# Kernel tuning notes

Measured on AMD Instinct MI355X. Metric: run time of the kernel, lower is better.

Reference implementation:

```python
import jax, jax.numpy as jnp
import numpy as np
import math

FACTOR = 3.0

def setup_inputs() -> dict:
    key = jax.random.key(0)
    k1, k2, k3 = jax.random.split(key, 3)
    B, L, H, E = 16, 4096, 8, 64
    queries = jax.random.normal(k1, (B, L, H, E), dtype=jnp.float32)
    keys = jax.random.normal(k2, (B, L, H, E), dtype=jnp.float32)
    values = jax.random.normal(k3, (B, L, H, E), dtype=jnp.float32)
    return {"queries": queries, "keys": keys, "values": values}

def reference(queries, keys, values):
    B, L, H, E = queries.shape
    top_k = int(FACTOR * math.log(L))  # 24 for L=4096 (static)
    # [B,H,E,L] layout for FFT along time
    q = jnp.transpose(queries, (0, 2, 3, 1))
    k = jnp.transpose(keys, (0, 2, 3, 1))
    v = jnp.transpose(values, (0, 2, 3, 1))
    # period-based autocorrelation via FFT cross-correlation
    qf = jnp.fft.rfft(q, axis=-1)
    kf = jnp.fft.rfft(k, axis=-1)
    corr = jnp.fft.irfft(qf * jnp.conj(kf), n=L, axis=-1)  # [B,H,E,L]
    # training-mode aggregation: shared top-k delay indices across batch
    mean_value = corr.mean(axis=(1, 2))                # [B,L]
    _, index = jax.lax.top_k(mean_value.mean(axis=0), top_k)  # [top_k]
    weights = mean_value[:, index]                     # [B,top_k]
    tmp_corr = jax.nn.softmax(weights, axis=-1)        # [B,top_k]
    delays_agg = jnp.zeros_like(v)
    for i in range(top_k):  # small static loop over delays
        pattern = jnp.roll(v, -index[i], axis=-1)
        delays_agg = delays_agg + pattern * tmp_corr[:, i][:, None, None, None]
    V = jnp.transpose(delays_agg, (0, 3, 1, 2))        # [B,L,H,E]
    return V
```

## Files before the change

### kernel.cpp

```cpp
#include <hip/hip_runtime.h>
#include <math.h>

#define B_ 16
#define L_ 4096
#define H_ 8
#define E_ 64
#define C_ 512
#define K_ 24
#define NT 256
#define RPAD 257

__device__ __forceinline__ int br12(int x) { return (int)(__brev((unsigned)x) >> 20); }

__device__ __forceinline__ float2 cmul(float2 a, float2 b) {
    return make_float2(a.x * b.x - a.y * b.y, a.x * b.y + a.y * b.x);
}
__device__ __forceinline__ float2 cadd(float2 a, float2 b) { return make_float2(a.x + b.x, a.y + b.y); }
__device__ __forceinline__ float2 csub(float2 a, float2 b) { return make_float2(a.x - b.x, a.y - b.y); }

__device__ __forceinline__ void bar_lds() {
    asm volatile("s_waitcnt lgkmcnt(0)" ::: "memory");
    __builtin_amdgcn_s_barrier();
}

__device__ __forceinline__ void fft16(float2 a[16]) {
    const float r2 = 0.70710678118654752f;
    const float c1 = 0.92387953251128676f;
    const float s1 = 0.38268343236508977f;
    const float2 W16[8] = {
        make_float2(1.f, 0.f),  make_float2(c1, -s1),  make_float2(r2, -r2),  make_float2(s1, -c1),
        make_float2(0.f, -1.f), make_float2(-s1, -c1), make_float2(-r2, -r2), make_float2(-c1, -s1)};
    #pragma unroll
    for (int j = 0; j < 8; ++j) {
        float2 u = a[j], v = a[j + 8];
        a[j]     = cadd(u, v);
        a[j + 8] = cmul(csub(u, v), W16[j]);
    }
    #pragma unroll
    for (int b = 0; b < 16; b += 8)
        #pragma unroll
        for (int j = 0; j < 4; ++j) {
            float2 u = a[b + j], v = a[b + j + 4];
            a[b + j]     = cadd(u, v);
            a[b + j + 4] = cmul(csub(u, v), W16[2 * j]);
        }
    #pragma unroll
    for (int b = 0; b < 16; b += 4)
        #pragma unroll
        for (int j = 0; j < 2; ++j) {
            float2 u = a[b + j], v = a[b + j + 2];
            a[b + j]     = cadd(u, v);
            a[b + j + 2] = cmul(csub(u, v), W16[4 * j]);
        }
    #pragma unroll
    for (int b = 0; b < 16; b += 2) {
        float2 u = a[b], v = a[b + 1];
        a[b]     = cadd(u, v);
        a[b + 1] = csub(u, v);
    }
}

__global__ __launch_bounds__(256) void k_zero(float* __restrict__ p, int n) {
    int i = blockIdx.x * 256 + threadIdx.x;
    if (i < n) p[i] = 0.f;
}

__global__ __launch_bounds__(256) void k_transpose(const float* __restrict__ q,
                                                   const float* __restrict__ k,
                                                   float2* __restrict__ z,
                                                   int b0) {
    __shared__ float tq[64][65];
    __shared__ float tk[64][65];
    int bl = blockIdx.z;
    int b  = b0 + bl;
    int t0 = blockIdx.x * 64;
    int c0 = blockIdx.y * 64;
    int tid  = threadIdx.x;
    int row  = tid >> 4;
    int col4 = (tid & 15) << 2;
    const size_t base = (size_t)b * L_ * C_;
    #pragma unroll
    for (int p = 0; p < 4; ++p) {
        int rr = (p << 4) + row;
        size_t off = base + (size_t)(t0 + rr) * C_ + (c0 + col4);
        float4 q4 = *(const float4*)(q + off);
        float4 k4 = *(const float4*)(k + off);
        tq[rr][col4 + 0] = q4.x; tq[rr][col4 + 1] = q4.y;
        tq[rr][col4 + 2] = q4.z; tq[rr][col4 + 3] = q4.w;
        tk[rr][col4 + 0] = k4.x; tk[rr][col4 + 1] = k4.y;
        tk[rr][col4 + 2] = k4.z; tk[rr][col4 + 3] = k4.w;
    }
    __syncthreads();
    #pragma unroll
    for (int p = 0; p < 4; ++p) {
        int cc = (p << 4) + row;
        int tg = col4;
        float4 w0 = make_float4(tq[tg + 0][cc], tk[tg + 0][cc],
                                tq[tg + 1][cc], tk[tg + 1][cc]);
        float4 w1 = make_float4(tq[tg + 2][cc], tk[tg + 2][cc],
                                tq[tg + 3][cc], tk[tg + 3][cc]);
        size_t zoff = ((size_t)bl * C_ + (c0 + cc)) * L_ + (t0 + tg);
        *(float4*)&z[zoff]     = w0;
        *(float4*)&z[zoff + 2] = w1;
    }
}

__global__ __launch_bounds__(256) void k_fft_accum(const float2* __restrict__ z,
                                                   float* __restrict__ cross,
                                                   int b0) {
    __shared__ float2 s[16 * RPAD];
    __shared__ float2 tw256[256];
    const int br4[16] = {0, 8, 4, 12, 2, 10, 6, 14, 1, 9, 5, 13, 3, 11, 7, 15};
    int t  = threadIdx.x;
    int bl = blockIdx.y;
    int b  = b0 + bl;
    int c0 = blockIdx.x * 8;

    {
        int r1 = t >> 4, m2 = t & 15;
        float sn, cs;
        sincospif((float)(r1 * m2) / 128.0f, &sn, &cs);
        tw256[t] = make_float2(cs, -sn);
    }
    float2 twA[15];
    #pragma unroll
    for (int k1 = 1; k1 < 16; ++k1) {
        float sn, cs;
        sincospif((float)(t * k1) / 2048.0f, &sn, &cs);
        twA[k1 - 1] = make_float2(cs, -sn);
    }
    float accx[16], accy[16];
    #pragma unroll
    for (int r = 0; r < 16; ++r) { accx[r] = 0.f; accy[r] = 0.f; }

    float2 a[16];
    {
        const float2* zc0 = z + ((size_t)bl * C_ + c0) * L_;
        #pragma unroll
        for (int j = 0; j < 16; ++j) a[j] = zc0[(j << 8) + t];
    }
    bar_lds();

    const int rowB = t >> 4, m2B = t & 15;
    const int k1C = t & 15, r1C = t >> 4;

    for (int cc = 0; cc < 8; ++cc) {
        fft16(a);
        #pragma unroll
        for (int k1 = 0; k1 < 16; ++k1) {
            float2 v = a[br4[k1]];
            if (k1) v = cmul(v, twA[k1 - 1]);
            s[k1 * RPAD + t] = v;
        }
        __syncthreads();
        #pragma unroll
        for (int m1 = 0; m1 < 16; ++m1) a[m1] = s[rowB * RPAD + (m1 << 4) + m2B];
        fft16(a);
        #pragma unroll
        for (int r1 = 0; r1 < 16; ++r1) {
            float2 v = cmul(a[br4[r1]], tw256[(r1 << 4) + m2B]);
            s[rowB * RPAD + (r1 << 4) + m2B] = v;
        }
        __syncthreads();
        #pragma unroll
        for (int m2 = 0; m2 < 16; ++m2) a[m2] = s[k1C * RPAD + (r1C << 4) + m2];
        fft16(a);
        __syncthreads();
        #pragma unroll
        for (int r2 = 0; r2 < 16; ++r2)
            s[(r2 << 8) + (r1C << 4) + k1C] = a[br4[r2]];
        if (cc < 7) {
            const float2* zn = z + ((size_t)bl * C_ + (c0 + cc + 1)) * L_;
            #pragma unroll
            for (int j = 0; j < 16; ++j) a[j] = zn[(j << 8) + t];
        }
        bar_lds();
        #pragma unroll
        for (int r = 0; r < 16; ++r) {
            int p  = t + (r << 8);
            int pp = (L_ - p) & (L_ - 1);
            float2 A  = s[p];
            float2 Bv = s[pp];
            float Qr = 0.5f * (A.x + Bv.x);
            float Qi = 0.5f * (A.y - Bv.y);
            float Kr = 0.5f * (A.y + Bv.y);
            float Ki = 0.5f * (A.x - Bv.x);
            accx[r] += Qr * Kr - Qi * Ki;
            accy[r] += Qr * Ki + Qi * Kr;
        }
        bar_lds();
    }
    #pragma unroll
    for (int r = 0; r < 16; ++r) {
        int p = t + (r << 8);
        atomicAdd(&cross[((size_t)b * L_ + p) * 2 + 0], accx[r]);
        atomicAdd(&cross[((size_t)b * L_ + p) * 2 + 1], accy[r]);
    }
}

__global__ __launch_bounds__(256) void k_ifft(const float* __restrict__ cross,
                                              float* __restrict__ mv) {
    __shared__ float2 s[L_];
    __shared__ float2 tw[L_ / 2];
    int tid = threadIdx.x;
    int b   = blockIdx.x;
    for (int j = tid; j < L_ / 2; j += NT) {
        float sn, cs;
        sincospif((float)j / 2048.0f, &sn, &cs);
        tw[j] = make_float2(cs, -sn);
    }
    const float2* cr = (const float2*)cross;
    #pragma unroll
    for (int r = 0; r < 16; ++r) {
        int p = tid + (r << 8);
        s[p] = cr[(size_t)b * L_ + br12(p)];
    }
    __syncthreads();
    for (int m = 1; m <= 12; ++m) {
        int half = 1 << (m - 1);
        #pragma unroll
        for (int t8 = 0; t8 < 8; ++t8) {
            int t  = tid + (t8 << 8);
            int kk = t & (half - 1);
            int i0 = ((t >> (m - 1)) << m) | kk;
            int i1 = i0 + half;
            float2 a = s[i0], bb = s[i1];
            float2 w = tw[kk << (12 - m)];
            float bwx = bb.x * w.x + bb.y * w.y;
            float bwy = bb.y * w.x - bb.x * w.y;
            s[i0] = make_float2(a.x + bwx, a.y + bwy);
            s[i1] = make_float2(a.x - bwx, a.y - bwy);
        }
        __syncthreads();
    }
    const float scale = 1.0f / ((float)L_ * (float)C_);
    #pragma unroll
    for (int r = 0; r < 16; ++r) {
        int p = tid + (r << 8);
        mv[(size_t)b * L_ + p] = s[p].x * scale;
    }
}

__global__ __launch_bounds__(256) void k_topk(const float* __restrict__ mv,
                                              int* __restrict__ idx,
                                              float* __restrict__ wts) {
    __shared__ float wv[4];
    __shared__ int   wi[4];
    __shared__ int   idxL[K_];
    int tid = threadIdx.x;
    float vloc[16];
    #pragma unroll
    for (int r = 0; r < 16; ++r) {
        int tt = tid + (r << 8);
        float ssum = 0.f;
        for (int b = 0; b < B_; ++b) ssum += mv[(size_t)b * L_ + tt];
        vloc[r] = ssum;
    }
    int lane = tid & 63, w = tid >> 6;
    for (int i = 0; i < K_; ++i) {
        float best = -INFINITY; int bi = 1 << 30;
        #pragma unroll
        for (int r = 0; r < 16; ++r) {
            float v = vloc[r]; int ii = tid + (r << 8);
            if (v > best || (v == best && ii < bi)) { best = v; bi = ii; }
        }
        #pragma unroll
        for (int off = 32; off > 0; off >>= 1) {
            float ov = __shfl_down(best, off);
            int   oi = __shfl_down(bi, off);
            if (ov > best || (ov == best && oi < bi)) { best = ov; bi = oi; }
        }
        if (lane == 0) { wv[w] = best; wi[w] = bi; }
        __syncthreads();
        if (tid == 0) {
            float bb = wv[0]; int bj = wi[0];
            for (int j = 1; j < 4; ++j)
                if (wv[j] > bb || (wv[j] == bb && wi[j] < bj)) { bb = wv[j]; bj = wi[j]; }
            idxL[i] = bj; idx[i] = bj;
        }
        __syncthreads();
        int win = idxL[i];
        #pragma unroll
        for (int r = 0; r < 16; ++r)
            if (win == tid + (r << 8)) vloc[r] = -INFINITY;
    }
    if (tid < B_) {
        int b = tid;
        float ww[K_]; float wm = -INFINITY;
        for (int i = 0; i < K_; ++i) { ww[i] = mv[(size_t)b * L_ + idxL[i]]; wm = fmaxf(wm, ww[i]); }
        float ssum = 0.f;
        for (int i = 0; i < K_; ++i) { ww[i] = expf(ww[i] - wm); ssum += ww[i]; }
        float inv = 1.f / ssum;
        for (int i = 0; i < K_; ++i) wts[b * K_ + i] = ww[i] * inv;
    }
}

__global__ __launch_bounds__(256) void k_agg(const float* __restrict__ vals,
                                             const int* __restrict__ idx,
                                             const float* __restrict__ wts,
                                             float* __restrict__ out) {
    __shared__ float4 sv[L_];
    __shared__ int   di[K_];
    __shared__ float dw[K_];
    const int tid = threadIdx.x;
    int id = blockIdx.x;
    int wk = ((id & 7) << 8) | (id >> 3);
    int b  = wk >> 7;
    int c0 = (wk & 127) << 2;

    if (tid < K_) { di[tid] = idx[tid]; dw[tid] = wts[b * K_ + tid]; }

    const float* gbase = vals + (size_t)b * L_ * C_ + c0;
    #pragma unroll
    for (int it = 0; it < 16; ++it) {
        int tau = (it << 8) + tid;
        const float* g = gbase + (size_t)tau * C_;
        float4* l = &sv[(it << 8) + ((tid >> 6) << 6)];
        __builtin_amdgcn_global_load_lds(
            (const __attribute__((address_space(1))) uint32_t*)g,
            (__attribute__((address_space(3))) uint32_t*)l,
            16, 0, 0);
    }
    __syncthreads();

    int   dir[K_]; float dwr[K_];
    #pragma unroll
    for (int i = 0; i < K_; ++i) { dir[i] = di[i]; dwr[i] = dw[i]; }

    float* obase = out + (size_t)b * L_ * C_ + c0;
    for (int r = 0; r < 16; ++r) {
        int tau = (r << 8) + tid;
        float4 acc = make_float4(0.f, 0.f, 0.f, 0.f);
        #pragma unroll
        for (int i = 0; i < K_; ++i) {
            float4 x = sv[(tau + dir[i]) & (L_ - 1)];
            float w = dwr[i];
            acc.x = fmaf(w, x.x, acc.x);
            acc.y = fmaf(w, x.y, acc.y);
            acc.z = fmaf(w, x.z, acc.z);
            acc.w = fmaf(w, x.w, acc.w);
        }
        *(float4*)(obase + (size_t)tau * C_) = acc;
    }
}

extern "C" void kernel_launch(void* const* d_in, const int* in_sizes, int n_in,
                              void* d_out, int out_size, void* d_ws, size_t ws_size,
                              hipStream_t stream) {
    const float* q = (const float*)d_in[0];
    const float* k = (const float*)d_in[1];
    const float* v = (const float*)d_in[2];
    float* out = (float*)d_out;
    char* ws = (char*)d_ws;

    float* cross = (float*)ws;
    float* mv    = (float*)(ws + (1 << 20));
    int*   idx   = (int*)(ws + (1 << 20) + (1 << 18));
    float* wts   = (float*)(ws + (1 << 20) + (1 << 18) + 4096);
    float2* z    = (float2*)(ws + (2 << 20));

    size_t zcap = (ws_size > (size_t)(2 << 20)) ? ws_size - (size_t)(2 << 20) : 0;
    int P = 16;
    while (P > 1 && (size_t)P * C_ * L_ * sizeof(float2) > zcap) P >>= 1;

    k_zero<<<(B_ * L_ * 2 + 255) / 256, 256, 0, stream>>>(cross, B_ * L_ * 2);

    for (int b0 = 0; b0 < B_; b0 += P) {
        dim3 gt(L_ / 64, C_ / 64, P);
        k_transpose<<<gt, 256, 0, stream>>>(q, k, z, b0);
        dim3 gf(C_ / 8, P);
        k_fft_accum<<<gf, 256, 0, stream>>>(z, cross, b0);
    }
    k_ifft<<<B_, 256, 0, stream>>>(cross, mv);
    k_topk<<<1, 256, 0, stream>>>(mv, idx, wts);
    k_agg<<<B_ * (C_ / 4) / 8 * 8, 256, 0, stream>>>(v, idx, wts, out);
}
```

Before: 379.6 us.

## Fuse first FFT radix-16 pass into transpose kernel and rewrite iFFT as radix-16

The transpose kernel now also performs the first radix-16 stage of the 4096-point FFT, including twiddle multiplication, before writing the intermediate to workspace. The accumulation kernel therefore starts at the second stage, which cuts its per-channel work and drops 15 sincos evaluations per thread. The per-batch inverse FFT changes from 12 radix-2 barrier-separated stages to a three-pass radix-16 scheme using conjugation. Twiddles are produced by repeated multiplication, which may add small rounding error, and the phaseA global stores are strided by 256 elements.

Result: faster. 361.1 us (-4.9%).

```diff
diff --git a/kernel.cpp b/kernel.cpp
--- a/kernel.cpp
+++ b/kernel.cpp
@@ -10,8 +10,6 @@
 #define NT 256
 #define RPAD 257
 
-__device__ __forceinline__ int br12(int x) { return (int)(__brev((unsigned)x) >> 20); }
-
 __device__ __forceinline__ float2 cmul(float2 a, float2 b) {
     return make_float2(a.x * b.x - a.y * b.y, a.x * b.y + a.y * b.x);
 }
@@ -65,49 +63,58 @@
     if (i < n) p[i] = 0.f;
 }
 
-__global__ __launch_bounds__(256) void k_transpose(const float* __restrict__ q,
-                                                   const float* __restrict__ k,
-                                                   float2* __restrict__ z,
-                                                   int b0) {
-    __shared__ float tq[64][65];
-    __shared__ float tk[64][65];
+__global__ __launch_bounds__(256) void k_phaseA(const float* __restrict__ q,
+                                                const float* __restrict__ k,
+                                                float2* __restrict__ z,
+                                                int b0) {
+    __shared__ float2 s2[256 * 17];
+    const int br4[16] = {0, 8, 4, 12, 2, 10, 6, 14, 1, 9, 5, 13, 3, 11, 7, 15};
+    int w  = blockIdx.x;
+    int g  = blockIdx.y;
     int bl = blockIdx.z;
     int b  = b0 + bl;
-    int t0 = blockIdx.x * 64;
-    int c0 = blockIdx.y * 64;
-    int tid  = threadIdx.x;
-    int row  = tid >> 4;
-    int col4 = (tid & 15) << 2;
-    const size_t base = (size_t)b * L_ * C_;
-    #pragma unroll
-    for (int p = 0; p < 4; ++p) {
-        int rr = (p << 4) + row;
-        size_t off = base + (size_t)(t0 + rr) * C_ + (c0 + col4);
-        float4 q4 = *(const float4*)(q + off);
-        float4 k4 = *(const float4*)(k + off);
-        tq[rr][col4 + 0] = q4.x; tq[rr][col4 + 1] = q4.y;
-        tq[rr][col4 + 2] = q4.z; tq[rr][col4 + 3] = q4.w;
-        tk[rr][col4 + 0] = k4.x; tk[rr][col4 + 1] = k4.y;
-        tk[rr][col4 + 2] = k4.z; tk[rr][col4 + 3] = k4.w;
+    int tid = threadIdx.x;
+
+    const size_t base = (size_t)b * L_ * C_ + g * 16;
+    int lrow = tid >> 2;
+    int lq   = tid & 3;
+    #pragma unroll
+    for (int it = 0; it < 4; ++it) {
+        int r   = lrow + (it << 6);
+        int tau = ((r >> 4) << 8) + (w << 4) + (r & 15);
+        const float4 q4 = *(const float4*)(q + base + (size_t)tau * C_ + (lq << 2));
+        const float4 k4 = *(const float4*)(k + base + (size_t)tau * C_ + (lq << 2));
+        float2* dst = &s2[r * 17 + (lq << 2)];
+        dst[0] = make_float2(q4.x, k4.x);
+        dst[1] = make_float2(q4.y, k4.y);
+        dst[2] = make_float2(q4.z, k4.z);
+        dst[3] = make_float2(q4.w, k4.w);
     }
     __syncthreads();
-    #pragma unroll
-    for (int p = 0; p < 4; ++p) {
-        int cc = (p << 4) + row;
-        int tg = col4;
-        float4 w0 = make_float4(tq[tg + 0][cc], tk[tg + 0][cc],
-                                tq[tg + 1][cc], tk[tg + 1][cc]);
-        float4 w1 = make_float4(tq[tg + 2][cc], tk[tg + 2][cc],
-                                tq[tg + 3][cc], tk[tg + 3][cc]);
-        size_t zoff = ((size_t)bl * C_ + (c0 + cc)) * L_ + (t0 + tg);
-        *(float4*)&z[zoff]     = w0;
-        *(float4*)&z[zoff + 2] = w1;
-    }
-}
-
-__global__ __launch_bounds__(256) void k_fft_accum(const float2* __restrict__ z,
-                                                   float* __restrict__ cross,
-                                                   int b0) {
+
+    int ch = tid >> 4, n2loc = tid & 15;
+    int n2 = (w << 4) + n2loc;
+    float2 a[16];
+    int rbase = n2loc * 17 + ch;
+    #pragma unroll
+    for (int n1 = 0; n1 < 16; ++n1) a[n1] = s2[n1 * 272 + rbase];
+    fft16(a);
+    float sn, cs;
+    sincospif((float)n2 / 2048.0f, &sn, &cs);
+    const float2 w1 = make_float2(cs, -sn);
+    float2 tw = w1;
+    float2* zc = z + ((size_t)bl * C_ + (g * 16 + ch)) * L_ + n2;
+    zc[0] = a[0];
+    #pragma unroll
+    for (int k1 = 1; k1 < 16; ++k1) {
+        zc[(size_t)(k1 << 8)] = cmul(a[br4[k1]], tw);
+        tw = cmul(tw, w1);
+    }
+}
+
+__global__ __launch_bounds__(256) void k_fft_bc(const float2* __restrict__ z,
+                                                float* __restrict__ cross,
+                                                int b0) {
     __shared__ float2 s[16 * RPAD];
     __shared__ float2 tw256[256];
     const int br4[16] = {0, 8, 4, 12, 2, 10, 6, 14, 1, 9, 5, 13, 3, 11, 7, 15};
@@ -122,45 +129,26 @@
         sincospif((float)(r1 * m2) / 128.0f, &sn, &cs);
         tw256[t] = make_float2(cs, -sn);
     }
-    float2 twA[15];
-    #pragma unroll
-    for (int k1 = 1; k1 < 16; ++k1) {
-        float sn, cs;
-        sincospif((float)(t * k1) / 2048.0f, &sn, &cs);
-        twA[k1 - 1] = make_float2(cs, -sn);
-    }
     float accx[16], accy[16];
     #pragma unroll
     for (int r = 0; r < 16; ++r) { accx[r] = 0.f; accy[r] = 0.f; }
+
+    const int rowB = t >> 4, m2B = t & 15;
+    const int k1C = t & 15, r1C = t >> 4;
 
     float2 a[16];
     {
         const float2* zc0 = z + ((size_t)bl * C_ + c0) * L_;
         #pragma unroll
-        for (int j = 0; j < 16; ++j) a[j] = zc0[(j << 8) + t];
+        for (int m1 = 0; m1 < 16; ++m1) a[m1] = zc0[(rowB << 8) + (m1 << 4) + m2B];
     }
     bar_lds();
-
-    const int rowB = t >> 4, m2B = t & 15;
-    const int k1C = t & 15, r1C = t >> 4;
 
     for (int cc = 0; cc < 8; ++cc) {
         fft16(a);
         #pragma unroll
-        for (int k1 = 0; k1 < 16; ++k1) {
-            float2 v = a[br4[k1]];
-            if (k1) v = cmul(v, twA[k1 - 1]);
-            s[k1 * RPAD + t] = v;
-        }
-        __syncthreads();
-        #pragma unroll
-        for (int m1 = 0; m1 < 16; ++m1) a[m1] = s[rowB * RPAD + (m1 << 4) + m2B];
-        fft16(a);
-        #pragma unroll
-        for (int r1 = 0; r1 < 16; ++r1) {
-            float2 v = cmul(a[br4[r1]], tw256[(r1 << 4) + m2B]);
-            s[rowB * RPAD + (r1 << 4) + m2B] = v;
-        }
+        for (int r1 = 0; r1 < 16; ++r1)
+            s[rowB * RPAD + (r1 << 4) + m2B] = cmul(a[br4[r1]], tw256[(r1 << 4) + m2B]);
         __syncthreads();
         #pragma unroll
         for (int m2 = 0; m2 < 16; ++m2) a[m2] = s[k1C * RPAD + (r1C << 4) + m2];
@@ -172,7 +160,7 @@
         if (cc < 7) {
             const float2* zn = z + ((size_t)bl * C_ + (c0 + cc + 1)) * L_;
             #pragma unroll
-            for (int j = 0; j < 16; ++j) a[j] = zn[(j << 8) + t];
+            for (int m1 = 0; m1 < 16; ++m1) a[m1] = zn[(rowB << 8) + (m1 << 4) + m2B];
         }
         bar_lds();
         #pragma unroll
@@ -200,45 +188,54 @@
 
 __global__ __launch_bounds__(256) void k_ifft(const float* __restrict__ cross,
                                               float* __restrict__ mv) {
-    __shared__ float2 s[L_];
-    __shared__ float2 tw[L_ / 2];
-    int tid = threadIdx.x;
-    int b   = blockIdx.x;
-    for (int j = tid; j < L_ / 2; j += NT) {
+    __shared__ float2 s[16 * RPAD];
+    __shared__ float2 tw256[256];
+    const int br4[16] = {0, 8, 4, 12, 2, 10, 6, 14, 1, 9, 5, 13, 3, 11, 7, 15};
+    int t = threadIdx.x;
+    int b = blockIdx.x;
+    {
+        int r1 = t >> 4, m2 = t & 15;
         float sn, cs;
-        sincospif((float)j / 2048.0f, &sn, &cs);
-        tw[j] = make_float2(cs, -sn);
-    }
-    const float2* cr = (const float2*)cross;
-    #pragma unroll
-    for (int r = 0; r < 16; ++r) {
-        int p = tid + (r << 8);
-        s[p] = cr[(size_t)b * L_ + br12(p)];
+        sincospif((float)(r1 * m2) / 128.0f, &sn, &cs);
+        tw256[t] = make_float2(cs, -sn);
+    }
+    const float2* cr = (const float2*)cross + (size_t)b * L_;
+    float2 a[16];
+    #pragma unroll
+    for (int n1 = 0; n1 < 16; ++n1) {
+        float2 v = cr[(n1 << 8) + t];
+        a[n1] = make_float2(v.x, -v.y);
+    }
+    fft16(a);
+    {
+        float sn, cs;
+        sincospif((float)t / 2048.0f, &sn, &cs);
+        const float2 w1 = make_float2(cs, -sn);
+        float2 tw = w1;
+        s[t] = a[0];
+        #pragma unroll
+        for (int k1 = 1; k1 < 16; ++k1) {
+            s[k1 * RPAD + t] = cmul(a[br4[k1]], tw);
+            tw = cmul(tw, w1);
+        }
     }
     __syncthreads();
-    for (int m = 1; m <= 12; ++m) {
-        int half = 1 << (m - 1);
-        #pragma unroll
-        for (int t8 = 0; t8 < 8; ++t8) {
-            int t  = tid + (t8 << 8);
-            int kk = t & (half - 1);
-            int i0 = ((t >> (m - 1)) << m) | kk;
-            int i1 = i0 + half;
-            float2 a = s[i0], bb = s[i1];
-            float2 w = tw[kk << (12 - m)];
-            float bwx = bb.x * w.x + bb.y * w.y;
-            float bwy = bb.y * w.x - bb.x * w.y;
-            s[i0] = make_float2(a.x + bwx, a.y + bwy);
-            s[i1] = make_float2(a.x - bwx, a.y - bwy);
-        }
-        __syncthreads();
-    }
+    const int rowB = t >> 4, m2B = t & 15;
+    #pragma unroll
+    for (int m1 = 0; m1 < 16; ++m1) a[m1] = s[rowB * RPAD + (m1 << 4) + m2B];
+    fft16(a);
+    #pragma unroll
+    for (int r1 = 0; r1 < 16; ++r1)
+        s[rowB * RPAD + (r1 << 4) + m2B] = cmul(a[br4[r1]], tw256[(r1 << 4) + m2B]);
+    __syncthreads();
+    const int k1C = t & 15, r1C = t >> 4;
+    #pragma unroll
+    for (int m2 = 0; m2 < 16; ++m2) a[m2] = s[k1C * RPAD + (r1C << 4) + m2];
+    fft16(a);
     const float scale = 1.0f / ((float)L_ * (float)C_);
     #pragma unroll
-    for (int r = 0; r < 16; ++r) {
-        int p = tid + (r << 8);
-        mv[(size_t)b * L_ + p] = s[p].x * scale;
-    }
+    for (int r2 = 0; r2 < 16; ++r2)
+        mv[(size_t)b * L_ + (r2 << 8) + t] = a[br4[r2]].x * scale;
 }
 
 __global__ __launch_bounds__(256) void k_topk(const float* __restrict__ mv,
@@ -366,10 +363,10 @@
     k_zero<<<(B_ * L_ * 2 + 255) / 256, 256, 0, stream>>>(cross, B_ * L_ * 2);
 
     for (int b0 = 0; b0 < B_; b0 += P) {
-        dim3 gt(L_ / 64, C_ / 64, P);
-        k_transpose<<<gt, 256, 0, stream>>>(q, k, z, b0);
-        dim3 gf(C_ / 8, P);
-        k_fft_accum<<<gf, 256, 0, stream>>>(z, cross, b0);
+        dim3 g1(16, 32, P);
+        k_phaseA<<<g1, 256, 0, stream>>>(q, k, z, b0);
+        dim3 g2(C_ / 8, P);
+        k_fft_bc<<<g2, 256, 0, stream>>>(z, cross, b0);
     }
     k_ifft<<<B_, 256, 0, stream>>>(cross, mv);
     k_topk<<<1, 256, 0, stream>>>(mv, idx, wts);
```
